# Optimization experiments

Measured on AMD Instinct MI355X. Metric: run time of the kernel, lower is better.

The kernel has to match this reference:

```python
import jax, jax.numpy as jnp
import numpy as np

B, S, D_MODEL = 2, 2048, 4096
N_HEADS, N_KV, HEAD_DIM = 32, 8, 128
N_GROUPS = N_HEADS // N_KV
QKV_DIM = (N_HEADS + 2 * N_KV) * HEAD_DIM


def _rope_tables(seq_len, head_dim, base=10000.0):
    inv_freq = 1.0 / (base ** (np.arange(0, head_dim, 2, dtype=np.float32) / head_dim))
    t = np.arange(seq_len, dtype=np.float32)
    freqs = np.outer(t, inv_freq)                      # [S, D/2]
    emb = np.concatenate([freqs, freqs], axis=-1)      # [S, D]
    return jnp.asarray(np.cos(emb)), jnp.asarray(np.sin(emb))


def setup_inputs() -> dict:
    key = jax.random.key(0)
    k1, k2, k3 = jax.random.split(key, 3)
    cos, sin = _rope_tables(S, HEAD_DIM)
    return {
        "hidden_states": jax.random.normal(k1, (B, S, D_MODEL), dtype=jnp.float32),
        "cos": cos,
        "sin": sin,
        "W_qkv": jax.random.normal(k2, (D_MODEL, QKV_DIM), dtype=jnp.float32) * (D_MODEL ** -0.5),
        "W_out": jax.random.normal(k3, (D_MODEL, D_MODEL), dtype=jnp.float32) * (D_MODEL ** -0.5),
    }


def _rotate_half(x):
    x1, x2 = jnp.split(x, 2, axis=-1)
    return jnp.concatenate([-x2, x1], axis=-1)


def _apply_rope(x, cos, sin):
    # x: [b, h, s, d]; cos/sin: [s, d]
    c = cos[None, None, :, :]
    s = sin[None, None, :, :]
    return x * c + _rotate_half(x) * s


def reference(hidden_states, cos, sin, W_qkv, W_out):
    b, s, _ = hidden_states.shape
    qkv = jnp.einsum("bsm,mq->bsq", hidden_states, W_qkv)
    q_end = N_HEADS * HEAD_DIM
    kv_sz = N_KV * HEAD_DIM
    q = qkv[..., :q_end].reshape(b, s, N_HEADS, HEAD_DIM).transpose(0, 2, 1, 3)
    k = qkv[..., q_end:q_end + kv_sz].reshape(b, s, N_KV, HEAD_DIM).transpose(0, 2, 1, 3)
    v = qkv[..., q_end + kv_sz:].reshape(b, s, N_KV, HEAD_DIM).transpose(0, 2, 1, 3)

    q = _apply_rope(q, cos, sin)          # [b, H, s, d]
    k = _apply_rope(k, cos, sin)          # [b, KV, s, d] (equiv. to repeat->rope->stride slice)

    # GQA without materializing repeated KV: group query heads per KV head.
    qg = q.reshape(b, N_KV, N_GROUPS, s, HEAD_DIM)
    scale = HEAD_DIM ** -0.5
    scores = jnp.einsum("bkgqd,bkpd->bkgqp", qg, k) * scale  # [b, KV, G, s, s]
    causal = jnp.tril(jnp.ones((s, s), dtype=bool))
    scores = jnp.where(causal, scores, jnp.finfo(scores.dtype).min)
    probs = jax.nn.softmax(scores, axis=-1)
    out = jnp.einsum("bkgqp,bkpd->bkgqd", probs, v)           # [b, KV, G, s, d]
    out = out.reshape(b, N_HEADS, s, HEAD_DIM).transpose(0, 2, 1, 3).reshape(b, s, D_MODEL)
    return jnp.einsum("bsm,mn->bsn", out, W_out)
```

## Files before the change

kernel.cpp:

```cpp
#include <hip/hip_runtime.h>


typedef __bf16 bf16;
typedef bf16 bf16x8 __attribute__((ext_vector_type(8)));
typedef bf16 bf16x4 __attribute__((ext_vector_type(4)));
typedef float f32x4 __attribute__((ext_vector_type(4)));
typedef unsigned int u32;
typedef u32 u32x4 __attribute__((ext_vector_type(4)));

#define B_ 2
#define S_ 2048
#define DM 4096
#define NH 32
#define NKV 8
#define HD 128
#define QKV_DIM 6144

typedef __attribute__((address_space(3))) void lds_void;
typedef const __attribute__((address_space(1))) void glb_void;

__device__ __forceinline__ void gld_lds16(const bf16* g, bf16* l) {
  __builtin_amdgcn_global_load_lds((glb_void*)g, (lds_void*)l, 16, 0, 0);
}

__device__ __forceinline__ u32 bf16bits(float x) {
  union { bf16 h; unsigned short s; } u;
  u.h = (bf16)x;
  return (u32)u.s;
}

#define BAR() __builtin_amdgcn_s_barrier()
#define VM4() asm volatile("s_waitcnt vmcnt(4)" ::: "memory")
#define VM0() asm volatile("s_waitcnt vmcnt(0)" ::: "memory")
#define PRIO1() __builtin_amdgcn_s_setprio(1)
#define PRIO0() __builtin_amdgcn_s_setprio(0)

__global__ __launch_bounds__(256) void cast_f32_bf16(const float* __restrict__ src,
                                                     bf16* __restrict__ dst, int n) {
  int i = (blockIdx.x * 256 + threadIdx.x) * 4;
  float4 v = *(const float4*)(src + i);
  bf16x4 o;
  o[0] = (bf16)v.x; o[1] = (bf16)v.y; o[2] = (bf16)v.z; o[3] = (bf16)v.w;
  *(bf16x4*)(dst + i) = o;
}

__global__ __launch_bounds__(256) void transpose_cast_w(const float* __restrict__ W,
                                                        bf16* __restrict__ Wt,
                                                        int K, int N) {
  __shared__ float tile[64][65];
  const int n0 = blockIdx.x * 64, k0 = blockIdx.y * 64;
  const int t = threadIdx.x, j = t & 63, i0 = t >> 6;
  for (int p = 0; p < 16; ++p) {
    int i = i0 + p * 4;
    tile[i][j] = W[(size_t)(k0 + i) * N + n0 + j];
  }
  __syncthreads();
  for (int p = 0; p < 16; ++p) {
    int n = i0 + p * 4;
    Wt[(size_t)(n0 + n) * K + k0 + j] = (bf16)tile[j][n];
  }
}

__global__ __launch_bounds__(256) void transpose_v(const bf16* __restrict__ qkv,
                                                   bf16* __restrict__ v_t) {
  __shared__ bf16 tile[64][65];
  const int s0 = blockIdx.x * 64;
  const int d0 = blockIdx.y * 64;
  const int bk = blockIdx.z;
  const int b = bk >> 3, kv = bk & 7;
  const int t = threadIdx.x, j = t & 63, i0 = t >> 6;
  const bf16* src = qkv + (size_t)b * S_ * QKV_DIM + 5120 + kv * HD;
  for (int p = 0; p < 16; ++p) {
    int i = i0 + p * 4;
    tile[i][j] = src[(size_t)(s0 + i) * QKV_DIM + d0 + j];
  }
  __syncthreads();
  bf16* dst = v_t + ((size_t)bk * HD + d0) * S_ + s0;
  for (int p = 0; p < 16; ++p) {
    int dd = i0 + p * 4;
    dst[(size_t)dd * S_ + j] = tile[j][dd];
  }
}

__global__ __launch_bounds__(128) void rope_kernel(const bf16* __restrict__ qkv,
                                                   const float* __restrict__ cosT,
                                                   const float* __restrict__ sinT,
                                                   bf16* __restrict__ q_r,
                                                   bf16* __restrict__ k_r) {
  const int bs = blockIdx.x;
  const int b = bs >> 11, s = bs & 2047;
  const int d = threadIdx.x;
  const float cv = cosT[s * HD + d];
  const float sv = sinT[s * HD + d];
  const bf16* row = qkv + (size_t)bs * QKV_DIM;
  const float scale = 0.08838834764831845f;
  for (int h = 0; h < NH; ++h) {
    float x = (float)row[h * HD + d];
    float xr = (d < 64) ? -(float)row[h * HD + d + 64] : (float)row[h * HD + d - 64];
    q_r[(((size_t)(b * NH + h)) * S_ + s) * HD + d] = (bf16)((x * cv + xr * sv) * scale);
  }
  for (int kv = 0; kv < NKV; ++kv) {
    float x = (float)row[DM + kv * HD + d];
    float xr = (d < 64) ? -(float)row[DM + kv * HD + d + 64] : (float)row[DM + kv * HD + d - 64];
    k_r[(((size_t)(b * NKV + kv)) * S_ + s) * HD + d] = (bf16)(x * cv + xr * sv);
  }
}

template <bool OUT_BF16, int BM, int BN>
__global__ __launch_bounds__(512, 2) void gemm_bt(const bf16* __restrict__ A,
                                                  const bf16* __restrict__ Bt,
                                                  void* __restrict__ Cout,
                                                  int M, int N, int K) {
  constexpr int MF = BM / 32;
  constexpr int NF = BN / 64;
  constexpr int NCA = BM / 128;
  constexpr int NCB = BN / 128;
  constexpr int AKH = BM * 64;
  constexpr int BKH = BN * 64;
  constexpr int BUF = 2 * (AKH + BKH);
  extern __shared__ char lds[];
  const int NT = K >> 6;

  const int nwg = gridDim.x;
  const int cpx = nwg >> 3;
  const int wg = (blockIdx.x & 7) * cpx + (blockIdx.x >> 3);
  const int nbx = N / BN;
  const int bx = wg % nbx, by = wg / nbx;
  const int m0 = by * BM, n0 = bx * BN;

  const int t = threadIdx.x;
  const int w = t >> 6, lane = t & 63;
  const int wr = w >> 2, wc = w & 3;
  const int quad = lane >> 4, c = lane & 15;

  const int aOff = (((wr * (BM / 2) + c) * 64 + quad * 16) ^ ((c & 8) << 2));
  const int bOff = 2 * AKH + ((((wc * (BN / 4) + c) * 64 + quad * 16) ^ ((c & 8) << 2)));

  const int scol = (((lane & 3) ^ ((lane >> 4) & 2)) << 3);
  const bf16* gA[NCA];
  const bf16* gB[NCB];
#pragma unroll
  for (int cc = 0; cc < NCA; ++cc)
    gA[cc] = A + (size_t)(m0 + w * (BM / 8) + cc * 16 + (lane >> 2)) * K + scol;
#pragma unroll
  for (int cc = 0; cc < NCB; ++cc)
    gB[cc] = Bt + (size_t)(n0 + w * (BN / 8) + cc * 16 + (lane >> 2)) * K + scol;

  auto stageKh = [&](int P, int kh, int ke) {
    char* ab = lds + P * BUF + kh * AKH + w * (BM * 8);
#pragma unroll
    for (int cc = 0; cc < NCA; ++cc) gld_lds16(gA[cc] + ke, (bf16*)(ab + cc * 1024));
    char* bb = lds + P * BUF + 2 * AKH + kh * BKH + w * (BN * 8);
#pragma unroll
    for (int cc = 0; cc < NCB; ++cc) gld_lds16(gB[cc] + ke, (bf16*)(bb + cc * 1024));
  };

  bf16x8 a0[MF], b0v[NF], a1[MF], b1v[NF];
  auto ldFr = [&](int P, int kh, bf16x8* av, bf16x8* bv) {
    const char* ab = lds + P * BUF + kh * AKH + aOff;
#pragma unroll
    for (int i = 0; i < MF; ++i) av[i] = *(const bf16x8*)(ab + i * 1024);
    const char* bb = lds + P * BUF + kh * BKH + bOff;
#pragma unroll
    for (int j = 0; j < NF; ++j) bv[j] = *(const bf16x8*)(bb + j * 1024);
  };

  f32x4 acc[MF][NF];
#pragma unroll
  for (int i = 0; i < MF; ++i)
#pragma unroll
    for (int j = 0; j < NF; ++j) acc[i][j] = (f32x4){0.f, 0.f, 0.f, 0.f};

  auto mfmac = [&](bf16x8* av, bf16x8* bv) {
    PRIO1();
#pragma unroll
    for (int i = 0; i < MF; ++i)
#pragma unroll
      for (int j = 0; j < NF; ++j)
        acc[i][j] = __builtin_amdgcn_mfma_f32_16x16x32_bf16(av[i], bv[j], acc[i][j], 0, 0, 0);
    PRIO0();
  };

  auto gtile = [&](int P, bool S0, bool S1) {
    BAR();
    ldFr(P, 0, a0, b0v);
    if (S0) stageKh(P ^ 1, 1, 96);
    mfmac(a0, b0v);
    ldFr(P, 1, a1, b1v);
    BAR();
    if (S1) stageKh(P, 0, 128);
    mfmac(a1, b1v);
  };

  auto adv = [&]() {
#pragma unroll
    for (int cc = 0; cc < NCA; ++cc) gA[cc] += 64;
#pragma unroll
    for (int cc = 0; cc < NCB; ++cc) gB[cc] += 64;
  };

  stageKh(0, 0, 0); stageKh(0, 1, 32); stageKh(1, 0, 64);
  VM4();

  for (int tt = 0; tt < NT - 2; tt += 2) {
    gtile(0, true, true); VM4(); adv();
    gtile(1, true, true); VM4(); adv();
  }
  gtile(0, true, false); VM0();
  gtile(1, false, false);

  const int crow = m0 + wr * (BM / 2) + quad * 4;
  const int ccol = n0 + wc * (BN / 4) + c;
#pragma unroll
  for (int mf = 0; mf < MF; ++mf)
#pragma unroll
    for (int nn = 0; nn < NF; ++nn) {
      const int row = crow + mf * 16;
      const int col = ccol + nn * 16;
      if constexpr (OUT_BF16) {
        bf16* Cp = (bf16*)Cout;
#pragma unroll
        for (int r = 0; r < 4; ++r) Cp[(size_t)(row + r) * N + col] = (bf16)acc[mf][nn][r];
      } else {
        float* Cp = (float*)Cout;
#pragma unroll
        for (int r = 0; r < 4; ++r) Cp[(size_t)(row + r) * N + col] = acc[mf][nn][r];
      }
    }
}

#define KVB 64
#define SKS 136
#define SVS 72
__global__ __launch_bounds__(256) void attn_kernel(const bf16* __restrict__ q_r,
                                                   const bf16* __restrict__ k_r,
                                                   const bf16* __restrict__ v_t,
                                                   bf16* __restrict__ attn_out) {
  __shared__ bf16 Ks[KVB * SKS];
  __shared__ bf16 Vs[128 * SVS];

  const int bh = blockIdx.x;
  const int b = bh >> 5, h = bh & 31;
  const int kv = h >> 2;
  const int q0 = blockIdx.y * 64;
  const int t = threadIdx.x, w = t >> 6, lane = t & 63;
  const int quad = lane >> 4, c = lane & 15;
  const int myq = q0 + w * 16 + c;

  const bf16* qrow = q_r + ((size_t)(b * NH + h) * S_ + myq) * HD;
  bf16x8 qf[4];
#pragma unroll
  for (int kk = 0; kk < 4; ++kk) qf[kk] = *(const bf16x8*)(qrow + quad * 8 + kk * 32);

  float m_i = -1e30f, l_i = 0.f;
  f32x4 o_acc[8];
#pragma unroll
  for (int n = 0; n < 8; ++n) o_acc[n] = (f32x4){0.f, 0.f, 0.f, 0.f};

  const bf16* kb_ptr = k_r + (size_t)(b * NKV + kv) * S_ * HD;
  const bf16* vb_ptr = v_t + (size_t)(b * NKV + kv) * HD * S_;

  const int nch = blockIdx.y + 1;

  const int kkey = t >> 2, kdoff = (t & 3) * 32;
  const int vd = t >> 1, vkoff = (t & 1) * 32;
  const bf16* kp = kb_ptr + (size_t)kkey * HD + kdoff;
  const bf16* vp = vb_ptr + (size_t)vd * S_ + vkoff;

  const int src0 = c + 32 * (quad & 1);
  const int src1 = src0 + 16;
  const bool hiTile = (quad & 2) != 0;

  auto packP = [&](const float* ea, const float* eb) -> bf16x8 {
    u32 pk[4];
#pragma unroll
    for (int r = 0; r < 4; ++r) pk[r] = bf16bits(ea[r]) | (bf16bits(eb[r]) << 16);
    u32 a0[4], a1[4];
#pragma unroll
    for (int r = 0; r < 4; ++r) {
      a0[r] = (u32)__shfl((int)pk[r], src0, 64);
      a1[r] = (u32)__shfl((int)pk[r], src1, 64);
    }
    u32 w0, w1, w2, w3;
    if (hiTile) {
      w0 = (a0[0] >> 16) | (a0[1] & 0xffff0000u);
      w1 = (a0[2] >> 16) | (a0[3] & 0xffff0000u);
      w2 = (a1[0] >> 16) | (a1[1] & 0xffff0000u);
      w3 = (a1[2] >> 16) | (a1[3] & 0xffff0000u);
    } else {
      w0 = (a0[0] & 0xffffu) | (a0[1] << 16);
      w1 = (a0[2] & 0xffffu) | (a0[3] << 16);
      w2 = (a1[0] & 0xffffu) | (a1[1] << 16);
      w3 = (a1[2] & 0xffffu) | (a1[3] << 16);
    }
    return __builtin_bit_cast(bf16x8, (u32x4){w0, w1, w2, w3});
  };

  bf16x8 krg[4], vrg[4];
#pragma unroll
  for (int i = 0; i < 4; ++i) {
    krg[i] = *(const bf16x8*)(kp + i * 8);
    vrg[i] = *(const bf16x8*)(vp + i * 8);
  }

  for (int ch = 0; ch < nch; ++ch) {
    const int kb = ch * KVB;
    __syncthreads();
#pragma unroll
    for (int i = 0; i < 4; ++i) {
      *(bf16x8*)(Ks + kkey * SKS + kdoff + i * 8) = krg[i];
      *(bf16x8*)(Vs + vd * SVS + vkoff + i * 8) = vrg[i];
    }
    if (ch + 1 < nch) {
      kp += (size_t)KVB * HD;
      vp += KVB;
#pragma unroll
      for (int i = 0; i < 4; ++i) {
        krg[i] = *(const bf16x8*)(kp + i * 8);
        vrg[i] = *(const bf16x8*)(vp + i * 8);
      }
    }
    __syncthreads();

    if (kb <= q0 + w * 16 + 15) {
      f32x4 st0 = (f32x4){0.f, 0.f, 0.f, 0.f};
      f32x4 st1 = (f32x4){0.f, 0.f, 0.f, 0.f};
      f32x4 st2 = (f32x4){0.f, 0.f, 0.f, 0.f};
      f32x4 st3 = (f32x4){0.f, 0.f, 0.f, 0.f};
#pragma unroll
      for (int kk = 0; kk < 4; ++kk) {
        bf16x8 kf0 = *(const bf16x8*)(Ks + (c) * SKS + quad * 8 + kk * 32);
        bf16x8 kf1 = *(const bf16x8*)(Ks + (16 + c) * SKS + quad * 8 + kk * 32);
        bf16x8 kf2 = *(const bf16x8*)(Ks + (32 + c) * SKS + quad * 8 + kk * 32);
        bf16x8 kf3 = *(const bf16x8*)(Ks + (48 + c) * SKS + quad * 8 + kk * 32);
        st0 = __builtin_amdgcn_mfma_f32_16x16x32_bf16(kf0, qf[kk], st0, 0, 0, 0);
        st1 = __builtin_amdgcn_mfma_f32_16x16x32_bf16(kf1, qf[kk], st1, 0, 0, 0);
        st2 = __builtin_amdgcn_mfma_f32_16x16x32_bf16(kf2, qf[kk], st2, 0, 0, 0);
        st3 = __builtin_amdgcn_mfma_f32_16x16x32_bf16(kf3, qf[kk], st3, 0, 0, 0);
      }

      float e0[4], e1[4], e2[4], e3[4];
#pragma unroll
      for (int r = 0; r < 4; ++r) { e0[r] = st0[r]; e1[r] = st1[r]; e2[r] = st2[r]; e3[r] = st3[r]; }
      if (kb + 63 > q0 + w * 16) {
        const int key0 = kb + quad * 4;
#pragma unroll
        for (int r = 0; r < 4; ++r) {
          if (key0 + r > myq) e0[r] = -1e30f;
          if (key0 + 16 + r > myq) e1[r] = -1e30f;
          if (key0 + 32 + r > myq) e2[r] = -1e30f;
          if (key0 + 48 + r > myq) e3[r] = -1e30f;
        }
      }

      float mloc = fmaxf(fmaxf(fmaxf(e0[0], e0[1]), fmaxf(e0[2], e0[3])),
                         fmaxf(fmaxf(e1[0], e1[1]), fmaxf(e1[2], e1[3])));
      mloc = fmaxf(mloc, fmaxf(fmaxf(fmaxf(e2[0], e2[1]), fmaxf(e2[2], e2[3])),
                               fmaxf(fmaxf(e3[0], e3[1]), fmaxf(e3[2], e3[3]))));
      mloc = fmaxf(mloc, __shfl_xor(mloc, 16, 64));
      mloc = fmaxf(mloc, __shfl_xor(mloc, 32, 64));
      const bool defer = (__all(mloc - m_i <= 8.0f) != 0);
      const float mnew = defer ? m_i : fmaxf(m_i, mloc);
      float sum = 0.f;
#pragma unroll
      for (int r = 0; r < 4; ++r) {
        e0[r] = __expf(e0[r] - mnew); sum += e0[r];
        e1[r] = __expf(e1[r] - mnew); sum += e1[r];
        e2[r] = __expf(e2[r] - mnew); sum += e2[r];
        e3[r] = __expf(e3[r] - mnew); sum += e3[r];
      }
      sum += __shfl_xor(sum, 16, 64);
      sum += __shfl_xor(sum, 32, 64);
      if (!defer) {
        const float alpha = __expf(m_i - mnew);
        m_i = mnew;
        l_i = l_i * alpha + sum;
        float alpha_o[4];
#pragma unroll
        for (int r = 0; r < 4; ++r) alpha_o[r] = __shfl(alpha, quad * 4 + r, 64);
#pragma unroll
        for (int n = 0; n < 8; ++n)
#pragma unroll
          for (int r = 0; r < 4; ++r) o_acc[n][r] *= alpha_o[r];
      } else {
        l_i += sum;
      }

      bf16x8 pf0 = packP(e0, e1);
      bf16x8 pf1 = packP(e2, e3);

#pragma unroll
      for (int n = 0; n < 8; ++n) {
        bf16x8 vf0 = *(const bf16x8*)(Vs + (n * 16 + c) * SVS + quad * 8);
        o_acc[n] = __builtin_amdgcn_mfma_f32_16x16x32_bf16(pf0, vf0, o_acc[n], 0, 0, 0);
        bf16x8 vf1 = *(const bf16x8*)(Vs + (n * 16 + c) * SVS + 32 + quad * 8);
        o_acc[n] = __builtin_amdgcn_mfma_f32_16x16x32_bf16(pf1, vf1, o_acc[n], 0, 0, 0);
      }
    }
  }

  float l_o[4];
#pragma unroll
  for (int r = 0; r < 4; ++r) l_o[r] = __shfl(l_i, quad * 4 + r, 64);
#pragma unroll
  for (int n = 0; n < 8; ++n)
#pragma unroll
    for (int r = 0; r < 4; ++r) {
      const int row = q0 + w * 16 + quad * 4 + r;
      const float ov = o_acc[n][r] / l_o[r];
      attn_out[((size_t)b * S_ + row) * DM + h * HD + n * 16 + c] = (bf16)ov;
    }
}

extern "C" void kernel_launch(void* const* d_in, const int* in_sizes, int n_in,
                              void* d_out, int out_size, void* d_ws, size_t ws_size,
                              hipStream_t stream) {
  const float* hidden = (const float*)d_in[0];
  const float* cosT = (const float*)d_in[1];
  const float* sinT = (const float*)d_in[2];
  const float* Wqkv = (const float*)d_in[3];
  const float* Wout = (const float*)d_in[4];
  float* out = (float*)d_out;
  char* ws = (char*)d_ws;

  bf16* WqkvT = (bf16*)(ws + 0);
  bf16* q_r = (bf16*)(ws + 0);
  bf16* k_r = (bf16*)(ws + 33554432);
  bf16* WoutT = (bf16*)(ws + 50331648);
  bf16* h_bf = (bf16*)(ws + 83886080);
  bf16* attn_out = (bf16*)(ws + 83886080);
  bf16* v_t = (bf16*)(ws + 117440512);
  bf16* qkv = (bf16*)d_out;

  static bool attr_set = false;
  if (!attr_set) {
    hipFuncSetAttribute(reinterpret_cast<const void*>(&gemm_bt<true, 128, 384>),
                        hipFuncAttributeMaxDynamicSharedMemorySize, 131072);
    hipFuncSetAttribute(reinterpret_cast<const void*>(&gemm_bt<false, 256, 256>),
                        hipFuncAttributeMaxDynamicSharedMemorySize, 131072);
    attr_set = true;
  }

  cast_f32_bf16<<<dim3(16384), dim3(256), 0, stream>>>(hidden, h_bf, B_ * S_ * DM);
  transpose_cast_w<<<dim3(QKV_DIM / 64, DM / 64), dim3(256), 0, stream>>>(Wqkv, WqkvT, DM, QKV_DIM);
  transpose_cast_w<<<dim3(DM / 64, DM / 64), dim3(256), 0, stream>>>(Wout, WoutT, DM, DM);
  gemm_bt<true, 128, 384><<<dim3((QKV_DIM / 384) * ((B_ * S_) / 128)), dim3(512), 131072, stream>>>(
      h_bf, WqkvT, (void*)qkv, B_ * S_, QKV_DIM, DM);
  rope_kernel<<<dim3(B_ * S_), dim3(128), 0, stream>>>(qkv, cosT, sinT, q_r, k_r);
  transpose_v<<<dim3(S_ / 64, HD / 64, B_ * NKV), dim3(256), 0, stream>>>(qkv, v_t);
  attn_kernel<<<dim3(B_ * NH, S_ / 64), dim3(256), 0, stream>>>(q_r, k_r, v_t, attn_out);
  gemm_bt<false, 256, 256><<<dim3((DM / 256) * ((B_ * S_) / 256)), dim3(512), 131072, stream>>>(
      attn_out, WoutT, (void*)out, B_ * S_, DM, DM);
}
```

Measured before the change: 793.9 us.

## Vectorize RoPE over all heads and enlarge attention query block to 128

RoPE now uses 320 threads per row, one group of eight elements per thread across all Q and K heads. It does 16-byte vector loads and stores, and reads the cos/sin tables as float4 instead of looping over heads with scalar accesses. The attention kernel moves to 128-query blocks with 8 waves and a swapped grid order, so each K/V tile staged in shared memory is reused by twice as many queries. Half-tiles that lie entirely above the causal diagonal now skip their QK, softmax and PV work. The larger blocks add registers and LDS pressure, and the causal load across blocks becomes less even.

```diff
diff --git a/kernel.cpp b/kernel.cpp
--- a/kernel.cpp
+++ b/kernel.cpp
@@ -82,28 +82,43 @@
   }
 }
 
-__global__ __launch_bounds__(128) void rope_kernel(const bf16* __restrict__ qkv,
+__global__ __launch_bounds__(320) void rope_kernel(const bf16* __restrict__ qkv,
                                                    const float* __restrict__ cosT,
                                                    const float* __restrict__ sinT,
                                                    bf16* __restrict__ q_r,
                                                    bf16* __restrict__ k_r) {
   const int bs = blockIdx.x;
   const int b = bs >> 11, s = bs & 2047;
-  const int d = threadIdx.x;
-  const float cv = cosT[s * HD + d];
-  const float sv = sinT[s * HD + d];
-  const bf16* row = qkv + (size_t)bs * QKV_DIM;
-  const float scale = 0.08838834764831845f;
-  for (int h = 0; h < NH; ++h) {
-    float x = (float)row[h * HD + d];
-    float xr = (d < 64) ? -(float)row[h * HD + d + 64] : (float)row[h * HD + d - 64];
-    q_r[(((size_t)(b * NH + h)) * S_ + s) * HD + d] = (bf16)((x * cv + xr * sv) * scale);
-  }
-  for (int kv = 0; kv < NKV; ++kv) {
-    float x = (float)row[DM + kv * HD + d];
-    float xr = (d < 64) ? -(float)row[DM + kv * HD + d + 64] : (float)row[DM + kv * HD + d - 64];
-    k_r[(((size_t)(b * NKV + kv)) * S_ + s) * HD + d] = (bf16)(x * cv + xr * sv);
-  }
+  const int t = threadIdx.x;
+  const int hh = t >> 3;
+  const int g = (t & 7) * 8;
+  const bool isQ = hh < NH;
+  const bf16* row = qkv + (size_t)bs * QKV_DIM + (isQ ? hh * HD : DM + (hh - NH) * HD);
+  bf16x8 xl8 = *(const bf16x8*)(row + g);
+  bf16x8 xh8 = *(const bf16x8*)(row + g + 64);
+  const float* cbase = cosT + (size_t)s * HD;
+  const float* sbase = sinT + (size_t)s * HD;
+  float cl[8], sl[8], ch[8], sh[8];
+  *(float4*)(cl) = *(const float4*)(cbase + g);
+  *(float4*)(cl + 4) = *(const float4*)(cbase + g + 4);
+  *(float4*)(ch) = *(const float4*)(cbase + g + 64);
+  *(float4*)(ch + 4) = *(const float4*)(cbase + g + 68);
+  *(float4*)(sl) = *(const float4*)(sbase + g);
+  *(float4*)(sl + 4) = *(const float4*)(sbase + g + 4);
+  *(float4*)(sh) = *(const float4*)(sbase + g + 64);
+  *(float4*)(sh + 4) = *(const float4*)(sbase + g + 68);
+  const float scale = isQ ? 0.08838834764831845f : 1.0f;
+  bf16x8 ol8, oh8;
+#pragma unroll
+  for (int j = 0; j < 8; ++j) {
+    const float xl = (float)xl8[j], xh = (float)xh8[j];
+    ol8[j] = (bf16)((xl * cl[j] - xh * sl[j]) * scale);
+    oh8[j] = (bf16)((xh * ch[j] + xl * sh[j]) * scale);
+  }
+  bf16* dst = isQ ? (q_r + (((size_t)(b * NH + hh)) * S_ + s) * HD)
+                  : (k_r + (((size_t)(b * NKV + (hh - NH))) * S_ + s) * HD);
+  *(bf16x8*)(dst + g) = ol8;
+  *(bf16x8*)(dst + g + 64) = oh8;
 }
 
 template <bool OUT_BF16, int BM, int BN>
@@ -229,20 +244,21 @@
     }
 }
 
+#define QBLK 128
 #define KVB 64
 #define SKS 136
 #define SVS 72
-__global__ __launch_bounds__(256) void attn_kernel(const bf16* __restrict__ q_r,
-                                                   const bf16* __restrict__ k_r,
-                                                   const bf16* __restrict__ v_t,
-                                                   bf16* __restrict__ attn_out) {
+__global__ __launch_bounds__(512, 4) void attn_kernel(const bf16* __restrict__ q_r,
+                                                      const bf16* __restrict__ k_r,
+                                                      const bf16* __restrict__ v_t,
+                                                      bf16* __restrict__ attn_out) {
   __shared__ bf16 Ks[KVB * SKS];
   __shared__ bf16 Vs[128 * SVS];
 
-  const int bh = blockIdx.x;
+  const int qb = blockIdx.x, bh = blockIdx.y;
   const int b = bh >> 5, h = bh & 31;
   const int kv = h >> 2;
-  const int q0 = blockIdx.y * 64;
+  const int q0 = qb * QBLK;
   const int t = threadIdx.x, w = t >> 6, lane = t & 63;
   const int quad = lane >> 4, c = lane & 15;
   const int myq = q0 + w * 16 + c;
@@ -260,12 +276,12 @@
   const bf16* kb_ptr = k_r + (size_t)(b * NKV + kv) * S_ * HD;
   const bf16* vb_ptr = v_t + (size_t)(b * NKV + kv) * HD * S_;
 
-  const int nch = blockIdx.y + 1;
-
-  const int kkey = t >> 2, kdoff = (t & 3) * 32;
-  const int vd = t >> 1, vkoff = (t & 1) * 32;
-  const bf16* kp = kb_ptr + (size_t)kkey * HD + kdoff;
-  const bf16* vp = vb_ptr + (size_t)vd * S_ + vkoff;
+  const int nch = 2 * qb + 2;
+
+  const int kkey = t >> 3, kg = (t & 7) * 8;
+  const int vd = t >> 2, vk = (t & 3) * 16;
+  const bf16* kp = kb_ptr + (size_t)kkey * HD + kg;
+  const bf16* vp = vb_ptr + (size_t)vd * S_ + vk;
 
   const int src0 = c + 32 * (quad & 1);
   const int src1 = src0 + 16;
@@ -296,33 +312,31 @@
     return __builtin_bit_cast(bf16x8, (u32x4){w0, w1, w2, w3});
   };
 
-  bf16x8 krg[4], vrg[4];
-#pragma unroll
-  for (int i = 0; i < 4; ++i) {
-    krg[i] = *(const bf16x8*)(kp + i * 8);
-    vrg[i] = *(const bf16x8*)(vp + i * 8);
-  }
+  bf16x8 krg0 = *(const bf16x8*)(kp);
+  bf16x8 krg1 = *(const bf16x8*)(kp + 64);
+  bf16x8 vrg0 = *(const bf16x8*)(vp);
+  bf16x8 vrg1 = *(const bf16x8*)(vp + 8);
 
   for (int ch = 0; ch < nch; ++ch) {
     const int kb = ch * KVB;
     __syncthreads();
-#pragma unroll
-    for (int i = 0; i < 4; ++i) {
-      *(bf16x8*)(Ks + kkey * SKS + kdoff + i * 8) = krg[i];
-      *(bf16x8*)(Vs + vd * SVS + vkoff + i * 8) = vrg[i];
-    }
+    *(bf16x8*)(Ks + kkey * SKS + kg) = krg0;
+    *(bf16x8*)(Ks + kkey * SKS + kg + 64) = krg1;
+    *(bf16x8*)(Vs + vd * SVS + vk) = vrg0;
+    *(bf16x8*)(Vs + vd * SVS + vk + 8) = vrg1;
     if (ch + 1 < nch) {
       kp += (size_t)KVB * HD;
       vp += KVB;
-#pragma unroll
-      for (int i = 0; i < 4; ++i) {
-        krg[i] = *(const bf16x8*)(kp + i * 8);
-        vrg[i] = *(const bf16x8*)(vp + i * 8);
-      }
+      krg0 = *(const bf16x8*)(kp);
+      krg1 = *(const bf16x8*)(kp + 64);
+      vrg0 = *(const bf16x8*)(vp);
+      vrg1 = *(const bf16x8*)(vp + 8);
     }
     __syncthreads();
 
-    if (kb <= q0 + w * 16 + 15) {
+    const int wmax = q0 + w * 16 + 15;
+    if (kb <= wmax) {
+      const bool hi = (kb + 32 <= wmax);
       f32x4 st0 = (f32x4){0.f, 0.f, 0.f, 0.f};
       f32x4 st1 = (f32x4){0.f, 0.f, 0.f, 0.f};
       f32x4 st2 = (f32x4){0.f, 0.f, 0.f, 0.f};
@@ -331,23 +345,33 @@
       for (int kk = 0; kk < 4; ++kk) {
         bf16x8 kf0 = *(const bf16x8*)(Ks + (c) * SKS + quad * 8 + kk * 32);
         bf16x8 kf1 = *(const bf16x8*)(Ks + (16 + c) * SKS + quad * 8 + kk * 32);
-        bf16x8 kf2 = *(const bf16x8*)(Ks + (32 + c) * SKS + quad * 8 + kk * 32);
-        bf16x8 kf3 = *(const bf16x8*)(Ks + (48 + c) * SKS + quad * 8 + kk * 32);
         st0 = __builtin_amdgcn_mfma_f32_16x16x32_bf16(kf0, qf[kk], st0, 0, 0, 0);
         st1 = __builtin_amdgcn_mfma_f32_16x16x32_bf16(kf1, qf[kk], st1, 0, 0, 0);
-        st2 = __builtin_amdgcn_mfma_f32_16x16x32_bf16(kf2, qf[kk], st2, 0, 0, 0);
-        st3 = __builtin_amdgcn_mfma_f32_16x16x32_bf16(kf3, qf[kk], st3, 0, 0, 0);
+      }
+      if (hi) {
+#pragma unroll
+        for (int kk = 0; kk < 4; ++kk) {
+          bf16x8 kf2 = *(const bf16x8*)(Ks + (32 + c) * SKS + quad * 8 + kk * 32);
+          bf16x8 kf3 = *(const bf16x8*)(Ks + (48 + c) * SKS + quad * 8 + kk * 32);
+          st2 = __builtin_amdgcn_mfma_f32_16x16x32_bf16(kf2, qf[kk], st2, 0, 0, 0);
+          st3 = __builtin_amdgcn_mfma_f32_16x16x32_bf16(kf3, qf[kk], st3, 0, 0, 0);
+        }
       }
 
       float e0[4], e1[4], e2[4], e3[4];
 #pragma unroll
       for (int r = 0; r < 4; ++r) { e0[r] = st0[r]; e1[r] = st1[r]; e2[r] = st2[r]; e3[r] = st3[r]; }
-      if (kb + 63 > q0 + w * 16) {
-        const int key0 = kb + quad * 4;
+      const int key0 = kb + quad * 4;
+      if (kb + 31 > q0 + w * 16) {
 #pragma unroll
         for (int r = 0; r < 4; ++r) {
           if (key0 + r > myq) e0[r] = -1e30f;
           if (key0 + 16 + r > myq) e1[r] = -1e30f;
+        }
+      }
+      if (hi && kb + 63 > q0 + w * 16) {
+#pragma unroll
+        for (int r = 0; r < 4; ++r) {
           if (key0 + 32 + r > myq) e2[r] = -1e30f;
           if (key0 + 48 + r > myq) e3[r] = -1e30f;
         }
@@ -355,8 +379,9 @@
 
       float mloc = fmaxf(fmaxf(fmaxf(e0[0], e0[1]), fmaxf(e0[2], e0[3])),
                          fmaxf(fmaxf(e1[0], e1[1]), fmaxf(e1[2], e1[3])));
-      mloc = fmaxf(mloc, fmaxf(fmaxf(fmaxf(e2[0], e2[1]), fmaxf(e2[2], e2[3])),
-                               fmaxf(fmaxf(e3[0], e3[1]), fmaxf(e3[2], e3[3]))));
+      if (hi)
+        mloc = fmaxf(mloc, fmaxf(fmaxf(fmaxf(e2[0], e2[1]), fmaxf(e2[2], e2[3])),
+                                 fmaxf(fmaxf(e3[0], e3[1]), fmaxf(e3[2], e3[3]))));
       mloc = fmaxf(mloc, __shfl_xor(mloc, 16, 64));
       mloc = fmaxf(mloc, __shfl_xor(mloc, 32, 64));
       const bool defer = (__all(mloc - m_i <= 8.0f) != 0);
@@ -366,8 +391,13 @@
       for (int r = 0; r < 4; ++r) {
         e0[r] = __expf(e0[r] - mnew); sum += e0[r];
         e1[r] = __expf(e1[r] - mnew); sum += e1[r];
-        e2[r] = __expf(e2[r] - mnew); sum += e2[r];
-        e3[r] = __expf(e3[r] - mnew); sum += e3[r];
+      }
+      if (hi) {
+#pragma unroll
+        for (int r = 0; r < 4; ++r) {
+          e2[r] = __expf(e2[r] - mnew); sum += e2[r];
+          e3[r] = __expf(e3[r] - mnew); sum += e3[r];
+        }
       }
       sum += __shfl_xor(sum, 16, 64);
       sum += __shfl_xor(sum, 32, 64);
@@ -387,14 +417,18 @@
       }
 
       bf16x8 pf0 = packP(e0, e1);
-      bf16x8 pf1 = packP(e2, e3);
-
 #pragma unroll
       for (int n = 0; n < 8; ++n) {
         bf16x8 vf0 = *(const bf16x8*)(Vs + (n * 16 + c) * SVS + quad * 8);
         o_acc[n] = __builtin_amdgcn_mfma_f32_16x16x32_bf16(pf0, vf0, o_acc[n], 0, 0, 0);
-        bf16x8 vf1 = *(const bf16x8*)(Vs + (n * 16 + c) * SVS + 32 + quad * 8);
-        o_acc[n] = __builtin_amdgcn_mfma_f32_16x16x32_bf16(pf1, vf1, o_acc[n], 0, 0, 0);
+      }
+      if (hi) {
+        bf16x8 pf1 = packP(e2, e3);
+#pragma unroll
+        for (int n = 0; n < 8; ++n) {
+          bf16x8 vf1 = *(const bf16x8*)(Vs + (n * 16 + c) * SVS + 32 + quad * 8);
+          o_acc[n] = __builtin_amdgcn_mfma_f32_16x16x32_bf16(pf1, vf1, o_acc[n], 0, 0, 0);
+        }
       }
     }
   }
@@ -446,9 +480,9 @@
   transpose_cast_w<<<dim3(DM / 64, DM / 64), dim3(256), 0, stream>>>(Wout, WoutT, DM, DM);
   gemm_bt<true, 128, 384><<<dim3((QKV_DIM / 384) * ((B_ * S_) / 128)), dim3(512), 131072, stream>>>(
       h_bf, WqkvT, (void*)qkv, B_ * S_, QKV_DIM, DM);
-  rope_kernel<<<dim3(B_ * S_), dim3(128), 0, stream>>>(qkv, cosT, sinT, q_r, k_r);
+  rope_kernel<<<dim3(B_ * S_), dim3(320), 0, stream>>>(qkv, cosT, sinT, q_r, k_r);
   transpose_v<<<dim3(S_ / 64, HD / 64, B_ * NKV), dim3(256), 0, stream>>>(qkv, v_t);
-  attn_kernel<<<dim3(B_ * NH, S_ / 64), dim3(256), 0, stream>>>(q_r, k_r, v_t, attn_out);
+  attn_kernel<<<dim3(S_ / QBLK, B_ * NH), dim3(512), 0, stream>>>(q_r, k_r, v_t, attn_out);
   gemm_bt<false, 256, 256><<<dim3((DM / 256) * ((B_ * S_) / 256)), dim3(512), 131072, stream>>>(
       attn_out, WoutT, (void*)out, B_ * S_, DM, DM);
 }
```

Result: slower. 829.1 us (+4.4%).
